# Kernel optimization log

Hardware: AMD Instinct MI355X
Metric: run time of the kernel (lower is better)

The kernel has to match this reference:

```python
import jax, jax.numpy as jnp
import numpy as np

H = 16  # number of heads (from init_kwargs)
LN_EPS = 1e-5  # torch nn.LayerNorm default


def layer_norm(x, g, b, eps=LN_EPS):
    mu = jnp.mean(x, axis=-1, keepdims=True)
    var = jnp.var(x, axis=-1, keepdims=True)
    return (x - mu) * jax.lax.rsqrt(var + eps) * g + b


def setup_inputs() -> dict:
    key = jax.random.key(0)
    ks = jax.random.split(key, 8)
    B, S, d = 2, 2048, 1024
    s = 0.02  # small init scale keeps softmax logits in a sane range
    return {
        "embed": jax.random.normal(ks[0], (B, S, d), jnp.float32),
        "Wk": jax.random.normal(ks[1], (d, d), jnp.float32) * s,
        "Wq": jax.random.normal(ks[2], (d, d), jnp.float32) * s,
        "Wv": jax.random.normal(ks[3], (d, d), jnp.float32) * s,
        "w1_w": jax.random.normal(ks[4], (4 * d, d), jnp.float32) * s,
        "w1_b": jnp.zeros((4 * d,), jnp.float32),
        "w2_w": jax.random.normal(ks[5], (d, 4 * d), jnp.float32) * s,
        "w2_b": jnp.zeros((d,), jnp.float32),
        "ln_g": jnp.ones((d,), jnp.float32),
        "ln_b": jnp.zeros((d,), jnp.float32),
        "ln2_g": jnp.ones((d,), jnp.float32),
        "ln2_b": jnp.zeros((d,), jnp.float32),
    }


def reference(embed, Wk, Wq, Wv, w1_w, w1_b, w2_w, w2_b, ln_g, ln_b, ln2_g, ln2_b):
    B, S, d = embed.shape
    dh = d // H
    # nn.Linear(d, d, bias=False): y = x @ W.T
    K = embed @ Wk.T
    Q = embed @ Wq.T
    V = embed @ Wv.T
    Qh = Q.reshape(B, S, H, dh)
    Kh = K.reshape(B, S, H, dh)
    Vh = V.reshape(B, S, H, dh)
    # per-head attention, all heads batched: [B, H, S, S]
    scores = jnp.einsum('bshd,bthd->bhst', Qh, Kh) / jnp.sqrt(jnp.float32(dh))
    attn = jax.nn.softmax(scores, axis=-1)
    out = jnp.einsum('bhst,bthd->bshd', attn, Vh).reshape(B, S, d)
    out = layer_norm(out + embed, ln_g, ln_b)          # residual + ln
    hidden = jax.nn.silu(out @ w1_w.T + w1_b)          # FFN with silu gate
    out2 = hidden @ w2_w.T + w2_b
    return layer_norm(out2 + out, ln2_g, ln2_b)        # residual + ln2
```

## Files before the change

kernel.cpp:

```cpp
#include <hip/hip_runtime.h>
#include <hip/hip_bf16.h>
#include <stdint.h>

typedef __attribute__((ext_vector_type(8))) __bf16 bf16x8;
typedef __attribute__((ext_vector_type(4))) float f32x4;
typedef __attribute__((ext_vector_type(16))) float f32x16;
typedef __attribute__((ext_vector_type(8))) uint16_t u16x8;

__device__ inline uint16_t f2bf(float x) {
  union { float f; uint32_t u; } v; v.f = x;
  uint32_t r = v.u + 0x7fffu + ((v.u >> 16) & 1u);
  return (uint16_t)(r >> 16);
}

#define MFMA16(a, b, c) __builtin_amdgcn_mfma_f32_16x16x32_bf16(a, b, c, 0, 0, 0)
#define MFMA32(a, b, c) __builtin_amdgcn_mfma_f32_32x32x16_bf16(a, b, c, 0, 0, 0)
#define GLOAD16(g, l) __builtin_amdgcn_global_load_lds((const __attribute__((address_space(1))) void*)(g), (__attribute__((address_space(3))) void*)(l), 16, 0, 0)

#if __has_builtin(__builtin_amdgcn_exp2f)
#define EXP2(x) __builtin_amdgcn_exp2f(x)
#else
#define EXP2(x) exp2f(x)
#endif

__device__ inline uint32_t cvtpk_bf16(float lo, float hi) {
  uint32_t r;
  asm("v_cvt_pk_bf16_f32 %0, %1, %2" : "=v"(r) : "v"(lo), "v"(hi));
  return r;
}
__device__ inline void perm32swap(uint32_t& a, uint32_t& b) {
  asm volatile("v_permlane32_swap_b32 %0, %1" : "+v"(a), "+v"(b));
}

__global__ void cast_all(const float* __restrict__ embed, const float* __restrict__ Wq,
                         const float* __restrict__ Wk, const float* __restrict__ Wv,
                         const float* __restrict__ w1w, const float* __restrict__ w2w,
                         uint16_t* __restrict__ xbf, uint16_t* __restrict__ wqkv,
                         uint16_t* __restrict__ w1b, uint16_t* __restrict__ w2b) {
  const int i = (blockIdx.x * 256 + threadIdx.x) * 4;
  const float* src; uint16_t* dst; float sc = 1.f; int off;
  if (i < 4194304)       { src = embed; dst = xbf;            off = i; }
  else if (i < 5242880)  { src = Wq;  dst = wqkv;             off = i - 4194304; sc = 0.125f * 1.44269504f; }
  else if (i < 6291456)  { src = Wk;  dst = wqkv + 1048576;   off = i - 5242880; }
  else if (i < 7340032)  { src = Wv;  dst = wqkv + 2097152;   off = i - 6291456; }
  else if (i < 11534336) { src = w1w; dst = w1b;              off = i - 7340032; }
  else                   { src = w2w; dst = w2b;              off = i - 11534336; }
  float4 v = *(const float4*)(src + off);
  ushort4 o;
  o.x = f2bf(v.x * sc); o.y = f2bf(v.y * sc);
  o.z = f2bf(v.z * sc); o.w = f2bf(v.w * sc);
  *(ushort4*)(dst + off) = o;
}

template <int EPI>
__global__ __launch_bounds__(512, 2) void gemm256(
    const uint16_t* __restrict__ A, const uint16_t* __restrict__ Bm,
    void* __restrict__ C0, void* __restrict__ C1, void* __restrict__ C2, void* __restrict__ C3,
    const float* __restrict__ bias, int N, int K, int ldk) {
  __shared__ uint16_t Als[2][256 * 64];
  __shared__ uint16_t Bls[2][256 * 64];
  const int tid = threadIdx.x;
  const int l = tid & 63, w = tid >> 6;
  const int wm = w >> 2, wn = w & 3;

  const int gx = gridDim.x;
  const int nwg = gx * gridDim.y;
  const int orig = blockIdx.y * gx + blockIdx.x;
  const int wg = (orig & 7) * (nwg >> 3) + (orig >> 3);
  const int row0 = (wg % gx) * 256;
  const int col0 = (wg / gx) * 256;

  const int kz = blockIdx.z;
  const uint16_t* Ap = A + (size_t)kz * K;
  const uint16_t* Bp = Bm + (size_t)kz * K;
  void* Co = kz == 0 ? C0 : (kz == 1 ? C1 : (kz == 2 ? C2 : C3));

  const int srow = w * 8 + (l >> 3);
  const int sgcol = ((l & 7) ^ (l >> 3)) * 8;

  auto STAGE = [&](int t) {
    const int buf = t & 1;
    const int kc = t * 64 + sgcol;
#pragma unroll
    for (int q = 0; q < 4; ++q) {
      GLOAD16(Ap + (size_t)(row0 + q * 64 + srow) * ldk + kc,
              (char*)&Als[buf][0] + q * 8192 + w * 1024);
      GLOAD16(Bp + (size_t)(col0 + q * 64 + srow) * ldk + kc,
              (char*)&Bls[buf][0] + q * 8192 + w * 1024);
    }
  };

  const int lr = l & 15;
  const int l4 = l >> 4;

  f32x4 acc[8][4] = {};
  bf16x8 a[4][2], b[4][2];

  auto LDA = [&](int buf, int mh) {
#pragma unroll
    for (int m = 0; m < 4; ++m) {
      const int r = wm * 128 + (mh * 4 + m) * 16 + lr;
#pragma unroll
      for (int kk = 0; kk < 2; ++kk)
        a[m][kk] = *(const bf16x8*)((const char*)&Als[buf][0] +
                     r * 128 + (((kk * 4 + l4) ^ (r & 7)) << 4));
    }
  };
  auto LDB = [&](int buf) {
#pragma unroll
    for (int n = 0; n < 4; ++n) {
      const int r = wn * 64 + n * 16 + lr;
#pragma unroll
      for (int kk = 0; kk < 2; ++kk)
        b[n][kk] = *(const bf16x8*)((const char*)&Bls[buf][0] +
                     r * 128 + (((kk * 4 + l4) ^ (r & 7)) << 4));
    }
  };

  const int nt = K >> 6;
  STAGE(0);
  STAGE(1);

#pragma unroll 1
  for (int t = 0; t < nt; ++t) {
    const int buf = t & 1;
    if (t < nt - 1) asm volatile("s_waitcnt vmcnt(8)" ::: "memory");
    else            asm volatile("s_waitcnt vmcnt(0)" ::: "memory");
    __builtin_amdgcn_s_barrier();

    LDB(buf);
    LDA(buf, 0);
    __builtin_amdgcn_s_setprio(1);
#pragma unroll
    for (int m = 0; m < 4; ++m)
#pragma unroll
      for (int n = 0; n < 4; ++n)
#pragma unroll
        for (int kk = 0; kk < 2; ++kk)
          acc[m][n] = MFMA16(a[m][kk], b[n][kk], acc[m][n]);
    __builtin_amdgcn_s_setprio(0);

    LDA(buf, 1);
    asm volatile("s_waitcnt lgkmcnt(0)" ::: "memory");
    __builtin_amdgcn_s_barrier();
    if (t + 2 < nt) STAGE(t + 2);

    __builtin_amdgcn_s_setprio(1);
#pragma unroll
    for (int m = 0; m < 4; ++m)
#pragma unroll
      for (int n = 0; n < 4; ++n)
#pragma unroll
        for (int kk = 0; kk < 2; ++kk)
          acc[4 + m][n] = MFMA16(a[m][kk], b[n][kk], acc[4 + m][n]);
    __builtin_amdgcn_s_setprio(0);
  }

  float bias_r[4];
  if (EPI != 0 && (EPI == 1 || kz == 0)) {
#pragma unroll
    for (int n = 0; n < 4; ++n) bias_r[n] = bias[col0 + wn * 64 + n * 16 + lr];
  }
#pragma unroll
  for (int m = 0; m < 8; ++m)
#pragma unroll
    for (int n = 0; n < 4; ++n)
#pragma unroll
      for (int v = 0; v < 4; ++v) {
        const int r = row0 + wm * 128 + m * 16 + ((l >> 4) << 2) + v;
        const int c = col0 + wn * 64 + n * 16 + lr;
        float x = acc[m][n][v];
        if (EPI == 0) {
          ((uint16_t*)Co)[(size_t)r * N + c] = f2bf(x);
        } else if (EPI == 1) {
          x += bias_r[n];
          float s = x / (1.f + __expf(-x));
          ((uint16_t*)Co)[(size_t)r * N + c] = f2bf(s);
        } else {
          if (kz == 0) x += bias_r[n];
          ((float*)Co)[(size_t)r * N + c] = x;
        }
      }
}

__global__ __launch_bounds__(256) void transpose_v(const uint16_t* __restrict__ qkv,
                                                   uint16_t* __restrict__ Vt) {
  __shared__ uint16_t t[64][72];
  const int kv0 = blockIdx.x * 64;
  const int bh = blockIdx.y;
  const size_t rowbase = (size_t)(bh >> 4) * 2048;
  const int hv = 2048 + (bh & 15) * 64;
  const int tid = threadIdx.x;
  const int r = tid >> 3, c8 = (tid & 7) * 8;
#pragma unroll
  for (int i = 0; i < 2; ++i) {
    const int row = i * 32 + r;
    u16x8 v = *(const u16x8*)(qkv + (rowbase + kv0 + row) * 3072 + hv + c8);
#pragma unroll
    for (int j = 0; j < 8; ++j) t[c8 + j][row] = v[j];
  }
  __syncthreads();
#pragma unroll
  for (int i = 0; i < 2; ++i) {
    const int d = i * 32 + r;
    u16x8 o;
#pragma unroll
    for (int j = 0; j < 8; ++j) o[j] = t[d][c8 + j];
    *(u16x8*)(Vt + ((size_t)bh * 64 + d) * 2048 + kv0 + c8) = o;
  }
}

__global__ __launch_bounds__(256, 2) void attn_kernel(const uint16_t* __restrict__ qkv,
                                                      const uint16_t* __restrict__ Vt,
                                                      float* __restrict__ out) {
  __shared__ uint16_t Klds[2][4096];
  __shared__ uint16_t Vlds[2][4096];
  const int tid = threadIdx.x;
  const int l = tid & 63, w = tid >> 6;
  const int lq = l & 31, hi = l >> 5;
  const int qt = blockIdx.x, bh = blockIdx.y;
  const size_t rowbase = (size_t)(bh >> 4) * 2048;
  const int h = bh & 15;
  const int hq = h * 64, hk = 1024 + h * 64;

  const int qrow = qt * 128 + w * 32 + lq;
  bf16x8 qf[4];
  {
    const uint16_t* qp = qkv + (rowbase + qrow) * 3072 + hq + hi * 8;
#pragma unroll
    for (int c = 0; c < 4; ++c) qf[c] = *(const bf16x8*)(qp + c * 16);
  }

  const int srow = w * 8 + (l >> 3);
  const int gcol = 8 * ((l & 7) ^ (l >> 3));

  f32x16 ot[2];
#pragma unroll
  for (int r = 0; r < 16; ++r) { ot[0][r] = 0.f; ot[1][r] = 0.f; }
  float m_run = -1e30f, l_run = 0.f;

  auto STAGE = [&](int buf, int kv0) {
#pragma unroll
    for (int p = 0; p < 2; ++p) {
      const uint16_t* srcK = qkv + (rowbase + kv0 + p * 32 + srow) * 3072 + hk + gcol;
      GLOAD16(srcK, (char*)&Klds[buf][0] + p * 4096 + w * 1024);
      const uint16_t* srcV = Vt + ((size_t)bh * 64 + p * 32 + srow) * 2048 + kv0 + gcol;
      GLOAD16(srcV, (char*)&Vlds[buf][0] + p * 4096 + w * 1024);
    }
  };

  STAGE(0, 0);
  int cur = 0;
  const int swz = (lq & 7) << 4;

  for (int t = 0; t < 32; ++t) {
    asm volatile("s_waitcnt vmcnt(0)" ::: "memory");
    __builtin_amdgcn_s_barrier();
    if (t < 31) STAGE(cur ^ 1, (t + 1) * 64);

    f32x16 st[2];
#pragma unroll
    for (int b = 0; b < 2; ++b) {
      f32x16 acm;
#pragma unroll
      for (int r = 0; r < 16; ++r) acm[r] = 0.f;
      __builtin_amdgcn_s_setprio(1);
#pragma unroll
      for (int c = 0; c < 4; ++c) {
        const int cbk = (c * 32 + hi * 16) ^ swz;
        bf16x8 kf = *(const bf16x8*)((const char*)&Klds[cur][0] + (b * 32 + lq) * 128 + cbk);
        acm = MFMA32(kf, qf[c], acm);
      }
      __builtin_amdgcn_s_setprio(0);
      st[b] = acm;
    }

    float mloc = st[0][0];
#pragma unroll
    for (int r = 1; r < 16; ++r) mloc = fmaxf(mloc, st[0][r]);
#pragma unroll
    for (int r = 0; r < 16; ++r) mloc = fmaxf(mloc, st[1][r]);
    const float mtile = fmaxf(mloc, __shfl_xor(mloc, 32, 64));
    if (!__all(mtile <= m_run + 8.f)) {
      const float mnew = fmaxf(m_run, mtile);
      const float sc = EXP2(m_run - mnew);
      m_run = mnew;
      l_run *= sc;
#pragma unroll
      for (int r = 0; r < 16; ++r) { ot[0][r] *= sc; ot[1][r] *= sc; }
    }
    float p0[16], p1[16];
    float rsum = 0.f;
#pragma unroll
    for (int r = 0; r < 16; ++r) { p0[r] = EXP2(st[0][r] - m_run); rsum += p0[r]; }
#pragma unroll
    for (int r = 0; r < 16; ++r) { p1[r] = EXP2(st[1][r] - m_run); rsum += p1[r]; }
    l_run += rsum + __shfl_xor(rsum, 32, 64);

    uint32_t pa[4][4];
#pragma unroll
    for (int b = 0; b < 2; ++b) {
      const float* pp = b ? p1 : p0;
#pragma unroll
      for (int c = 0; c < 2; ++c) {
        uint32_t a0 = cvtpk_bf16(pp[8 * c + 0], pp[8 * c + 1]);
        uint32_t a1 = cvtpk_bf16(pp[8 * c + 2], pp[8 * c + 3]);
        uint32_t b0 = cvtpk_bf16(pp[8 * c + 4], pp[8 * c + 5]);
        uint32_t b1 = cvtpk_bf16(pp[8 * c + 6], pp[8 * c + 7]);
        perm32swap(a0, b0);
        perm32swap(a1, b1);
        pa[b * 2 + c][0] = a0; pa[b * 2 + c][1] = a1;
        pa[b * 2 + c][2] = b0; pa[b * 2 + c][3] = b1;
      }
    }

    __builtin_amdgcn_s_setprio(1);
#pragma unroll
    for (int ks = 0; ks < 4; ++ks) {
      bf16x8 pf = *(bf16x8*)&pa[ks][0];
#pragma unroll
      for (int db = 0; db < 2; ++db) {
        const int cbk = (ks * 32 + hi * 16) ^ swz;
        bf16x8 vf = *(const bf16x8*)((const char*)&Vlds[cur][0] + (db * 32 + lq) * 128 + cbk);
        ot[db] = MFMA32(vf, pf, ot[db]);
      }
    }
    __builtin_amdgcn_s_setprio(0);
    cur ^= 1;
  }

  const float linv = 1.f / l_run;
  float* orow = out + (rowbase + qrow) * 1024 + h * 64;
#pragma unroll
  for (int db = 0; db < 2; ++db)
#pragma unroll
    for (int m = 0; m < 4; ++m) {
      float4 v;
      v.x = ot[db][4 * m + 0] * linv;
      v.y = ot[db][4 * m + 1] * linv;
      v.z = ot[db][4 * m + 2] * linv;
      v.w = ot[db][4 * m + 3] * linv;
      *(float4*)(orow + db * 32 + 8 * m + 4 * hi) = v;
    }
}

__global__ __launch_bounds__(256) void ln_kernel(const float* __restrict__ x0p,
                                                 const float* __restrict__ x1p,
                                                 const float* __restrict__ x2p,
                                                 const float* __restrict__ x3p,
                                                 const float* __restrict__ x4p,
                                                 const float* __restrict__ g,
                                                 const float* __restrict__ b,
                                                 float* __restrict__ y32,
                                                 uint16_t* __restrict__ y16) {
  const int row = blockIdx.x;
  const int t = threadIdx.x;
  const int l = t & 63, w = t >> 6;
  float4 va = *((const float4*)(x0p + (size_t)row * 1024) + t);
  float4 vb = *((const float4*)(x1p + (size_t)row * 1024) + t);
  float x0 = va.x + vb.x, x1 = va.y + vb.y, x2 = va.z + vb.z, x3 = va.w + vb.w;
  if (x2p) {
    float4 vc = *((const float4*)(x2p + (size_t)row * 1024) + t);
    x0 += vc.x; x1 += vc.y; x2 += vc.z; x3 += vc.w;
  }
  if (x3p) {
    float4 vc = *((const float4*)(x3p + (size_t)row * 1024) + t);
    x0 += vc.x; x1 += vc.y; x2 += vc.z; x3 += vc.w;
  }
  if (x4p) {
    float4 vc = *((const float4*)(x4p + (size_t)row * 1024) + t);
    x0 += vc.x; x1 += vc.y; x2 += vc.z; x3 += vc.w;
  }
  float s = x0 + x1 + x2 + x3;
  float q = x0 * x0 + x1 * x1 + x2 * x2 + x3 * x3;
#pragma unroll
  for (int off = 1; off < 64; off <<= 1) {
    s += __shfl_xor(s, off, 64);
    q += __shfl_xor(q, off, 64);
  }
  __shared__ float red[8];
  if (l == 0) { red[w] = s; red[w + 4] = q; }
  __syncthreads();
  s = red[0] + red[1] + red[2] + red[3];
  q = red[4] + red[5] + red[6] + red[7];
  const float mu = s * (1.f / 1024.f);
  const float var = q * (1.f / 1024.f) - mu * mu;
  const float rstd = rsqrtf(var + 1e-5f);
  float4 vg = *((const float4*)g + t);
  float4 vbb = *((const float4*)b + t);
  float y0 = (x0 - mu) * rstd * vg.x + vbb.x;
  float y1 = (x1 - mu) * rstd * vg.y + vbb.y;
  float y2 = (x2 - mu) * rstd * vg.z + vbb.z;
  float y3 = (x3 - mu) * rstd * vg.w + vbb.w;
  *((float4*)(y32 + (size_t)row * 1024) + t) = make_float4(y0, y1, y2, y3);
  if (y16) {
    union { uint16_t u[4]; uint64_t v; } o;
    o.u[0] = f2bf(y0); o.u[1] = f2bf(y1); o.u[2] = f2bf(y2); o.u[3] = f2bf(y3);
    *((uint64_t*)(y16 + (size_t)row * 1024) + t) = o.v;
  }
}

extern "C" void kernel_launch(void* const* d_in, const int* in_sizes, int n_in,
                              void* d_out, int out_size, void* d_ws, size_t ws_size,
                              hipStream_t stream) {
  const float* embed = (const float*)d_in[0];
  const float* Wk = (const float*)d_in[1];
  const float* Wq = (const float*)d_in[2];
  const float* Wv = (const float*)d_in[3];
  const float* w1w = (const float*)d_in[4];
  const float* w1bias = (const float*)d_in[5];
  const float* w2w = (const float*)d_in[6];
  const float* w2bias = (const float*)d_in[7];
  const float* lng = (const float*)d_in[8];
  const float* lnb = (const float*)d_in[9];
  const float* ln2g = (const float*)d_in[10];
  const float* ln2b = (const float*)d_in[11];

  char* ws = (char*)d_ws;
  uint16_t* qkv  = (uint16_t*)(ws);
  uint16_t* xbf  = (uint16_t*)(ws + 25165824);
  uint16_t* wqkv = (uint16_t*)(ws + 33554432);
  uint16_t* w1b  = (uint16_t*)(ws + 39845888);
  uint16_t* w2b  = (uint16_t*)(ws + 48234496);
  float*    attf = (float*)(ws + 56623104);
  float*    yf   = (float*)(ws + 73400320);
  uint16_t* hid  = (uint16_t*)(ws + 90177536);
  uint16_t* Vt   = (uint16_t*)(ws + 90177536);
  float*    part1 = (float*)qkv;
  float*    part2 = (float*)(ws + 25165824);
  float*    part3 = (float*)d_out;

  cast_all<<<dim3(15360), dim3(256), 0, stream>>>(embed, Wq, Wk, Wv, w1w, w2w,
                                                  xbf, wqkv, w1b, w2b);

  gemm256<0><<<dim3(16, 12), dim3(512), 0, stream>>>(xbf, wqkv, qkv, nullptr, nullptr, nullptr,
                                                     nullptr, 3072, 1024, 1024);
  transpose_v<<<dim3(32, 32), dim3(256), 0, stream>>>(qkv, Vt);
  attn_kernel<<<dim3(16, 32), dim3(256), 0, stream>>>(qkv, Vt, attf);
  ln_kernel<<<dim3(4096), dim3(256), 0, stream>>>(attf, embed, nullptr, nullptr, nullptr,
                                                  lng, lnb, yf, xbf);
  gemm256<1><<<dim3(16, 16), dim3(512), 0, stream>>>(xbf, w1b, hid, nullptr, nullptr, nullptr,
                                                     w1bias, 4096, 1024, 1024);
  gemm256<2><<<dim3(16, 4, 4), dim3(512), 0, stream>>>(hid, w2b, attf, part1, part2, part3,
                                                       w2bias, 1024, 1024, 4096);
  ln_kernel<<<dim3(4096), dim3(256), 0, stream>>>(attf, part1, part2, part3, yf,
                                                  ln2g, ln2b, (float*)d_out, nullptr);
}
```

Measured before the change: 214.2 us.

## Split GEMM main loop into four MFMA quadrants interleaved with LDS reads and staging

Splits the B fragment into two halves and the per-iteration MFMA work into four 4x2 quadrants. LDS reads and the global-to-LDS staging of the next A and B tiles are interleaved between the quadrants with extra barriers, in a ping-pong style schedule. The aim is to overlap LDS and global load latency with matrix math and to lower fragment register pressure. The cost is more barriers per iteration. Issuing STAGE_B into the buffer still being read relies on that buffer's reads having finished, and this holds only if the barrier placement is correct.

```diff
diff --git a/kernel.cpp b/kernel.cpp
--- a/kernel.cpp
+++ b/kernel.cpp
@@ -78,23 +78,28 @@
   const int srow = w * 8 + (l >> 3);
   const int sgcol = ((l & 7) ^ (l >> 3)) * 8;
 
-  auto STAGE = [&](int t) {
+  auto STAGE_A = [&](int t) {
     const int buf = t & 1;
     const int kc = t * 64 + sgcol;
 #pragma unroll
-    for (int q = 0; q < 4; ++q) {
+    for (int q = 0; q < 4; ++q)
       GLOAD16(Ap + (size_t)(row0 + q * 64 + srow) * ldk + kc,
               (char*)&Als[buf][0] + q * 8192 + w * 1024);
+  };
+  auto STAGE_B = [&](int t) {
+    const int buf = t & 1;
+    const int kc = t * 64 + sgcol;
+#pragma unroll
+    for (int q = 0; q < 4; ++q)
       GLOAD16(Bp + (size_t)(col0 + q * 64 + srow) * ldk + kc,
               (char*)&Bls[buf][0] + q * 8192 + w * 1024);
-    }
   };
 
   const int lr = l & 15;
   const int l4 = l >> 4;
 
   f32x4 acc[8][4] = {};
-  bf16x8 a[4][2], b[4][2];
+  bf16x8 a[4][2], b0[2][2], b1[2][2];
 
   auto LDA = [&](int buf, int mh) {
 #pragma unroll
@@ -106,20 +111,30 @@
                      r * 128 + (((kk * 4 + l4) ^ (r & 7)) << 4));
     }
   };
-  auto LDB = [&](int buf) {
-#pragma unroll
-    for (int n = 0; n < 4; ++n) {
-      const int r = wn * 64 + n * 16 + lr;
+  auto LDB = [&](int buf, int nh, bf16x8 (&bb)[2][2]) {
+#pragma unroll
+    for (int n = 0; n < 2; ++n) {
+      const int r = wn * 64 + (nh * 2 + n) * 16 + lr;
 #pragma unroll
       for (int kk = 0; kk < 2; ++kk)
-        b[n][kk] = *(const bf16x8*)((const char*)&Bls[buf][0] +
+        bb[n][kk] = *(const bf16x8*)((const char*)&Bls[buf][0] +
                      r * 128 + (((kk * 4 + l4) ^ (r & 7)) << 4));
     }
   };
 
+#define MM8(MO, NO, BB)                                                          \
+  {                                                                              \
+    __builtin_amdgcn_s_setprio(1);                                               \
+    _Pragma("unroll") for (int m = 0; m < 4; ++m)                                \
+      _Pragma("unroll") for (int n = 0; n < 2; ++n)                              \
+        _Pragma("unroll") for (int kk = 0; kk < 2; ++kk)                         \
+          acc[MO + m][NO + n] = MFMA16(a[m][kk], BB[n][kk], acc[MO + m][NO + n]); \
+    __builtin_amdgcn_s_setprio(0);                                               \
+  }
+
   const int nt = K >> 6;
-  STAGE(0);
-  STAGE(1);
+  STAGE_A(0); STAGE_B(0);
+  STAGE_A(1); STAGE_B(1);
 
 #pragma unroll 1
   for (int t = 0; t < nt; ++t) {
@@ -128,32 +143,22 @@
     else            asm volatile("s_waitcnt vmcnt(0)" ::: "memory");
     __builtin_amdgcn_s_barrier();
 
-    LDB(buf);
+    LDB(buf, 0, b0);
     LDA(buf, 0);
-    __builtin_amdgcn_s_setprio(1);
-#pragma unroll
-    for (int m = 0; m < 4; ++m)
-#pragma unroll
-      for (int n = 0; n < 4; ++n)
-#pragma unroll
-        for (int kk = 0; kk < 2; ++kk)
-          acc[m][n] = MFMA16(a[m][kk], b[n][kk], acc[m][n]);
-    __builtin_amdgcn_s_setprio(0);
+    MM8(0, 0, b0)
+    __builtin_amdgcn_s_barrier();
+
+    LDB(buf, 1, b1);
+    MM8(0, 2, b1)
+    __builtin_amdgcn_s_barrier();
 
     LDA(buf, 1);
-    asm volatile("s_waitcnt lgkmcnt(0)" ::: "memory");
+    if (t + 2 < nt) STAGE_B(t + 2);
+    MM8(4, 2, b1)
     __builtin_amdgcn_s_barrier();
-    if (t + 2 < nt) STAGE(t + 2);
-
-    __builtin_amdgcn_s_setprio(1);
-#pragma unroll
-    for (int m = 0; m < 4; ++m)
-#pragma unroll
-      for (int n = 0; n < 4; ++n)
-#pragma unroll
-        for (int kk = 0; kk < 2; ++kk)
-          acc[4 + m][n] = MFMA16(a[m][kk], b[n][kk], acc[4 + m][n]);
-    __builtin_amdgcn_s_setprio(0);
+
+    if (t + 2 < nt) STAGE_A(t + 2);
+    MM8(4, 0, b0)
   }
 
   float bias_r[4];
```

Result: no change. 213.0 us (-0.6%).
